# Kernel optimization log

Hardware: AMD Instinct MI355X
Metric: run time of the kernel (lower is better)

The kernel has to match this reference:

```python
import jax, jax.numpy as jnp
import numpy as np

N = 100000
E = 3200000
IN_CH = 512
H1 = 16


def setup_inputs() -> dict:
    key = jax.random.key(0)
    ks = jax.random.split(key, 9)
    x = jax.random.normal(ks[0], (N, IN_CH), dtype=jnp.float32)
    edge_index = jax.random.randint(ks[1], (2, E), 0, N, dtype=jnp.int64)
    # GCNConv params: weight [in, out], bias [out]
    def glorot(k, fan_in, fan_out):
        lim = (6.0 / (fan_in + fan_out)) ** 0.5
        return jax.random.uniform(k, (fan_in, fan_out), jnp.float32, -lim, lim)
    W1 = glorot(ks[2], IN_CH, H1)
    b1 = jnp.zeros((H1,), jnp.float32)
    W2 = glorot(ks[3], H1, H1)
    b2 = jnp.zeros((H1,), jnp.float32)
    W3 = glorot(ks[4], H1, 1)
    b3 = jnp.zeros((1,), jnp.float32)
    return {"x": x, "edge_index": edge_index, "W1": W1, "b1": b1,
            "W2": W2, "b2": b2, "W3": W3, "b3": b3}


def _gcn_conv(x, W, b, src, dst, deg_isqrt):
    # GCNConv: h = X W; out = D^-1/2 (A + I) D^-1/2 h + b
    h = x @ W  # [N, out]
    norm = deg_isqrt[src] * deg_isqrt[dst]  # [E]
    msg = h[src] * norm[:, None]  # gather + scale
    agg = jax.ops.segment_sum(msg, dst, num_segments=N)  # scatter-add
    agg = agg + h * (deg_isqrt * deg_isqrt)[:, None]  # self-loop term
    return agg + b


def reference(x, edge_index, W1, b1, W2, b2, W3, b3):
    src, dst = edge_index[0], edge_index[1]
    # degree of A + I, counted on destination nodes (symmetric norm)
    deg = jax.ops.segment_sum(jnp.ones((E,), jnp.float32), dst, num_segments=N) + 1.0
    deg_isqrt = jax.lax.rsqrt(deg)
    h = _gcn_conv(x, W1, b1, src, dst, deg_isqrt)
    h = jax.nn.relu(h)  # dropout is identity at eval
    h = _gcn_conv(h, W2, b2, src, dst, deg_isqrt)
    h = jax.nn.relu(h)
    out = _gcn_conv(h, W3, b3, src, dst, deg_isqrt)
    return out
```

## Files before the change

kernel.cpp:

```cpp
#include <hip/hip_runtime.h>
#include <hip/hip_bf16.h>

static constexpr int N_NODES = 100000;
static constexpr int N_EDGES = 3200000;
static constexpr int IN_CH = 512;
static constexpr int H = 16;
static constexpr int TB = 256;

static constexpr int BN = 256;
static constexpr int NB = (N_NODES + BN - 1) / BN;
static constexpr int CAP = 8960;
static constexpr int CAP2 = CAP + 3 * BN;
static constexpr int CHUNK = 8192;
static constexpr int GRID_SC = (N_EDGES + CHUNK - 1) / CHUNK;
static constexpr int NBLK64 = (N_NODES + 63) / 64;

__global__ void k_init(int* __restrict__ gcur) {
  int b = blockIdx.x * blockDim.x + threadIdx.x;
  if (b < NB) gcur[b] = b * CAP;
}

__global__ void k_cscatter(const int* __restrict__ ei, int* __restrict__ gcur,
                           int* __restrict__ ebuf) {
  __shared__ int cnt[NB];
  __shared__ int gofs[NB];
  int t = threadIdx.x;
  int c0 = blockIdx.x * CHUNK;
  int c1 = min(c0 + CHUNK, N_EDGES);
  for (int b = t; b < NB; b += TB) cnt[b] = 0;
  __syncthreads();
  for (int j = c0 + t; j < c1; j += TB) atomicAdd(&cnt[ei[N_EDGES + j] >> 8], 1);
  __syncthreads();
  for (int b = t; b < NB; b += TB)
    if (cnt[b] > 0) gofs[b] = atomicAdd(&gcur[b], cnt[b]);
  __syncthreads();
  for (int j = c0 + t; j < c1; j += TB) {
    int s = ei[j];
    int d = ei[N_EDGES + j];
    int slot = atomicAdd(&gofs[d >> 8], 1);
    ebuf[slot] = ((d & 255) << 17) | s;
  }
}

__global__ void k_bsort(const int* __restrict__ gcur, const int* __restrict__ ebuf,
                        int* __restrict__ ebuf2, int* __restrict__ nrs,
                        int* __restrict__ nend, float* __restrict__ disq) {
  __shared__ int cnt[BN];
  __shared__ int pre[BN];
  __shared__ int cur[BN];
  int b = blockIdx.x, t = threadIdx.x;
  cnt[t] = 0;
  __syncthreads();
  int beg = b * CAP, end = gcur[b];
  for (int j = beg + t; j < end; j += TB) atomicAdd(&cnt[ebuf[j] >> 17], 1);
  __syncthreads();
  int myc = cnt[t];
  int ac = (myc + 3) & ~3;
  pre[t] = ac;
  __syncthreads();
  for (int off = 1; off < TB; off <<= 1) {
    int v = (t >= off) ? pre[t - off] : 0;
    __syncthreads();
    pre[t] += v;
    __syncthreads();
  }
  int start = b * CAP2 + ((t == 0) ? 0 : pre[t - 1]);
  cur[t] = start;
  int node = b * BN + t;
  if (node < N_NODES) {
    nrs[node] = start;
    nend[node] = start + ac;
    disq[node] = 1.0f / sqrtf((float)myc + 1.0f);
    for (int j = start + myc; j < start + ac; j++) ebuf2[j] = N_NODES;
  }
  __syncthreads();
  for (int j = beg + t; j < end; j += TB) {
    int p = ebuf[j];
    int slot = atomicAdd(&cur[p >> 17], 1);
    ebuf2[slot] = p & 0x1FFFF;
  }
}

__global__ void k_gemm1(const float* __restrict__ x, const float* __restrict__ W,
                        const float* __restrict__ disq,
                        float* __restrict__ hloA, float* __restrict__ hhiA,
                        float* __restrict__ hloB, float* __restrict__ hhiB,
                        float* __restrict__ hs3) {
  int r = blockIdx.x * blockDim.x + threadIdx.x;
  if (r > N_NODES) return;
  if (r == N_NODES) {
    float4 z = make_float4(0.f, 0.f, 0.f, 0.f);
    ((float4*)(hloA + (size_t)r * 8))[0] = z;
    ((float4*)(hloA + (size_t)r * 8))[1] = z;
    ((float4*)(hhiA + (size_t)r * 8))[0] = z;
    ((float4*)(hhiA + (size_t)r * 8))[1] = z;
    ((float4*)(hloB + (size_t)r * 8))[0] = z;
    ((float4*)(hloB + (size_t)r * 8))[1] = z;
    ((float4*)(hhiB + (size_t)r * 8))[0] = z;
    ((float4*)(hhiB + (size_t)r * 8))[1] = z;
    hs3[r] = 0.f;
    return;
  }
  const float4* xr = (const float4*)(x + (size_t)r * IN_CH);
  float acc[H];
#pragma unroll
  for (int c = 0; c < H; c++) acc[c] = 0.f;
  for (int k4 = 0; k4 < IN_CH / 4; k4++) {
    float4 xv = xr[k4];
    const float* wr = W + k4 * 4 * H;
    float xs[4] = {xv.x, xv.y, xv.z, xv.w};
#pragma unroll
    for (int j = 0; j < 4; j++) {
#pragma unroll
      for (int c = 0; c < H; c++) acc[c] = fmaf(xs[j], wr[j * H + c], acc[c]);
    }
  }
  float dn = disq[r];
  float4* lo = (float4*)(hloA + (size_t)r * 8);
  float4* hi = (float4*)(hhiA + (size_t)r * 8);
  lo[0] = make_float4(acc[0] * dn, acc[1] * dn, acc[2] * dn, acc[3] * dn);
  lo[1] = make_float4(acc[4] * dn, acc[5] * dn, acc[6] * dn, acc[7] * dn);
  hi[0] = make_float4(acc[8] * dn, acc[9] * dn, acc[10] * dn, acc[11] * dn);
  hi[1] = make_float4(acc[12] * dn, acc[13] * dn, acc[14] * dn, acc[15] * dn);
}

__global__ void k_gath_mid(const int* __restrict__ nrs, const int* __restrict__ nend,
                           const int* __restrict__ ebuf2, const float* __restrict__ disq,
                           const float* __restrict__ inlo, const float* __restrict__ inhi,
                           const float* __restrict__ W2, const float* __restrict__ bias,
                           float* __restrict__ outlo, float* __restrict__ outhi) {
  __shared__ float agg[64 * 16];
  __shared__ float w[256];
  int b = blockIdx.x, t = threadIdx.x;
  w[t] = W2[t];
  int grp = t >> 3, lane = t & 7;
#pragma unroll
  for (int ph = 0; ph < 2; ph++) {
    const float* hs = ph ? inhi : inlo;
#pragma unroll
    for (int k = 0; k < 2; k++) {
      int node = b * 64 + grp * 2 + k;
      if (node < N_NODES) {
        int beg = nrs[node], endp = nend[node];
        float acc = 0.f;
        for (int j = beg; j < endp; j += 4) {
          int4 s = *(const int4*)(ebuf2 + j);
          float a0 = hs[(size_t)s.x * 8 + lane];
          float a1 = hs[(size_t)s.y * 8 + lane];
          float a2 = hs[(size_t)s.z * 8 + lane];
          float a3 = hs[(size_t)s.w * 8 + lane];
          acc += (a0 + a1) + (a2 + a3);
        }
        float dn = disq[node];
        agg[(grp * 2 + k) * 16 + ph * 8 + lane] =
            fmaf(acc + hs[(size_t)node * 8 + lane], dn, bias[ph * 8 + lane]);
      }
    }
  }
  __syncthreads();
  int nl = t >> 2, q = t & 3;
  int node = b * 64 + nl;
  if (node < N_NODES) {
    float o0 = 0.f, o1 = 0.f, o2 = 0.f, o3 = 0.f;
#pragma unroll
    for (int c4 = 0; c4 < 4; c4++) {
      float4 av = *(const float4*)(agg + nl * 16 + c4 * 4);
      float vs[4] = {av.x, av.y, av.z, av.w};
#pragma unroll
      for (int i2 = 0; i2 < 4; i2++) {
        float v = fmaxf(vs[i2], 0.f);
        const float* wr = w + (c4 * 4 + i2) * 16 + q * 4;
        o0 = fmaf(v, wr[0], o0);
        o1 = fmaf(v, wr[1], o1);
        o2 = fmaf(v, wr[2], o2);
        o3 = fmaf(v, wr[3], o3);
      }
    }
    float dn = disq[node];
    float4 r = make_float4(o0 * dn, o1 * dn, o2 * dn, o3 * dn);
    if (q < 2) *(float4*)(outlo + (size_t)node * 8 + q * 4) = r;
    else *(float4*)(outhi + (size_t)node * 8 + (q - 2) * 4) = r;
  }
}

__global__ void k_gath_last(const int* __restrict__ nrs, const int* __restrict__ nend,
                            const int* __restrict__ ebuf2, const float* __restrict__ disq,
                            const float* __restrict__ inlo, const float* __restrict__ inhi,
                            const float* __restrict__ W3, const float* __restrict__ bias,
                            float* __restrict__ hs3) {
  __shared__ float agg[64 * 16];
  __shared__ float w3[16];
  int b = blockIdx.x, t = threadIdx.x;
  if (t < 16) w3[t] = W3[t];
  int grp = t >> 3, lane = t & 7;
#pragma unroll
  for (int ph = 0; ph < 2; ph++) {
    const float* hs = ph ? inhi : inlo;
#pragma unroll
    for (int k = 0; k < 2; k++) {
      int node = b * 64 + grp * 2 + k;
      if (node < N_NODES) {
        int beg = nrs[node], endp = nend[node];
        float acc = 0.f;
        for (int j = beg; j < endp; j += 4) {
          int4 s = *(const int4*)(ebuf2 + j);
          float a0 = hs[(size_t)s.x * 8 + lane];
          float a1 = hs[(size_t)s.y * 8 + lane];
          float a2 = hs[(size_t)s.z * 8 + lane];
          float a3 = hs[(size_t)s.w * 8 + lane];
          acc += (a0 + a1) + (a2 + a3);
        }
        float dn = disq[node];
        agg[(grp * 2 + k) * 16 + ph * 8 + lane] =
            fmaf(acc + hs[(size_t)node * 8 + lane], dn, bias[ph * 8 + lane]);
      }
    }
  }
  __syncthreads();
  int nl = t >> 2, q = t & 3;
  int node = b * 64 + nl;
  if (node < N_NODES) {
    float4 av = *(const float4*)(agg + nl * 16 + q * 4);
    float o = fmaxf(av.x, 0.f) * w3[q * 4 + 0];
    o = fmaf(fmaxf(av.y, 0.f), w3[q * 4 + 1], o);
    o = fmaf(fmaxf(av.z, 0.f), w3[q * 4 + 2], o);
    o = fmaf(fmaxf(av.w, 0.f), w3[q * 4 + 3], o);
    o += __shfl_xor(o, 1);
    o += __shfl_xor(o, 2);
    if (q == 0) hs3[node] = o * disq[node];
  }
}

__global__ void k_gath1(const int* __restrict__ nrs, const int* __restrict__ nend,
                        const int* __restrict__ ebuf2, const float* __restrict__ disq,
                        const float* __restrict__ hs3, const float* __restrict__ bias,
                        float* __restrict__ out) {
  int b = blockIdx.x, t = threadIdx.x;
  int nl = t >> 2, lane = t & 3;
  int node = b * 64 + nl;
  if (node >= N_NODES) return;
  int beg = nrs[node], endp = nend[node];
  float acc = 0.f;
  for (int j = beg + 4 * lane; j < endp; j += 16) {
    int4 s = *(const int4*)(ebuf2 + j);
    acc += (hs3[s.x] + hs3[s.y]) + (hs3[s.z] + hs3[s.w]);
  }
  acc += __shfl_xor(acc, 1);
  acc += __shfl_xor(acc, 2);
  if (lane == 0) out[node] = fmaf(acc + hs3[node], disq[node], bias[0]);
}

extern "C" void kernel_launch(void* const* d_in, const int* in_sizes, int n_in,
                              void* d_out, int out_size, void* d_ws, size_t ws_size,
                              hipStream_t stream) {
  const float* x = (const float*)d_in[0];
  const int* ei = (const int*)d_in[1];
  const float* W1 = (const float*)d_in[2];
  const float* b1 = (const float*)d_in[3];
  const float* W2 = (const float*)d_in[4];
  const float* b2 = (const float*)d_in[5];
  const float* W3 = (const float*)d_in[6];
  const float* b3 = (const float*)d_in[7];
  float* out = (float*)d_out;

  int* ebuf = (int*)d_ws;
  int* ebuf2 = ebuf + (size_t)NB * CAP;
  int* gcur = ebuf2 + (size_t)NB * CAP2;
  int* nrs = gcur + NB;
  int* nend = nrs + N_NODES;
  int pad = (4 - ((NB + 2 * N_NODES) & 3)) & 3;
  float* disq = (float*)(nend + N_NODES + pad);
  float* hloA = disq + N_NODES;
  float* hhiA = hloA + (size_t)(N_NODES + 1) * 8;
  float* hloB = hhiA + (size_t)(N_NODES + 1) * 8;
  float* hhiB = hloB + (size_t)(N_NODES + 1) * 8;
  float* hs3 = hhiB + (size_t)(N_NODES + 1) * 8;

  k_init<<<(NB + 63) / 64, 64, 0, stream>>>(gcur);
  k_cscatter<<<GRID_SC, TB, 0, stream>>>(ei, gcur, ebuf);
  k_bsort<<<NB, TB, 0, stream>>>(gcur, ebuf, ebuf2, nrs, nend, disq);

  k_gemm1<<<(N_NODES + 64) / 64, 64, 0, stream>>>(x, W1, disq, hloA, hhiA, hloB, hhiB, hs3);
  k_gath_mid<<<NBLK64, TB, 0, stream>>>(nrs, nend, ebuf2, disq, hloA, hhiA, W2, b1, hloB, hhiB);
  k_gath_last<<<NBLK64, TB, 0, stream>>>(nrs, nend, ebuf2, disq, hloB, hhiB, W3, b2, hs3);
  k_gath1<<<NBLK64, TB, 0, stream>>>(nrs, nend, ebuf2, disq, hs3, b3, out);
}
```

Before: 552.3 us.

## Store 16-wide features contiguously and gather float4 per lane in one pass

Replaces the split lo/hi 8-float feature arrays with a single contiguous 16-float row per node. The gather kernels now have 4 lanes per node, each loading a float4 per neighbor in one pass, instead of 8 lanes doing scalar loads over two phases. Each neighbor row becomes one 64-byte access, and the edge list is walked once instead of twice. The last layer no longer stages results in shared memory or synchronises. In exchange each thread handles more work per edge, with fewer threads per node and less parallelism per edge list.

Result: no change. 557.2 us (+0.9%).

```diff
diff --git a/kernel.cpp b/kernel.cpp
--- a/kernel.cpp
+++ b/kernel.cpp
@@ -83,21 +83,16 @@
 
 __global__ void k_gemm1(const float* __restrict__ x, const float* __restrict__ W,
                         const float* __restrict__ disq,
-                        float* __restrict__ hloA, float* __restrict__ hhiA,
-                        float* __restrict__ hloB, float* __restrict__ hhiB,
+                        float* __restrict__ hA, float* __restrict__ hB,
                         float* __restrict__ hs3) {
   int r = blockIdx.x * blockDim.x + threadIdx.x;
   if (r > N_NODES) return;
+  float4* oa = (float4*)(hA + (size_t)r * 16);
   if (r == N_NODES) {
     float4 z = make_float4(0.f, 0.f, 0.f, 0.f);
-    ((float4*)(hloA + (size_t)r * 8))[0] = z;
-    ((float4*)(hloA + (size_t)r * 8))[1] = z;
-    ((float4*)(hhiA + (size_t)r * 8))[0] = z;
-    ((float4*)(hhiA + (size_t)r * 8))[1] = z;
-    ((float4*)(hloB + (size_t)r * 8))[0] = z;
-    ((float4*)(hloB + (size_t)r * 8))[1] = z;
-    ((float4*)(hhiB + (size_t)r * 8))[0] = z;
-    ((float4*)(hhiB + (size_t)r * 8))[1] = z;
+    float4* ob = (float4*)(hB + (size_t)r * 16);
+#pragma unroll
+    for (int i = 0; i < 4; i++) { oa[i] = z; ob[i] = z; }
     hs3[r] = 0.f;
     return;
   }
@@ -116,55 +111,53 @@
     }
   }
   float dn = disq[r];
-  float4* lo = (float4*)(hloA + (size_t)r * 8);
-  float4* hi = (float4*)(hhiA + (size_t)r * 8);
-  lo[0] = make_float4(acc[0] * dn, acc[1] * dn, acc[2] * dn, acc[3] * dn);
-  lo[1] = make_float4(acc[4] * dn, acc[5] * dn, acc[6] * dn, acc[7] * dn);
-  hi[0] = make_float4(acc[8] * dn, acc[9] * dn, acc[10] * dn, acc[11] * dn);
-  hi[1] = make_float4(acc[12] * dn, acc[13] * dn, acc[14] * dn, acc[15] * dn);
+  oa[0] = make_float4(acc[0] * dn, acc[1] * dn, acc[2] * dn, acc[3] * dn);
+  oa[1] = make_float4(acc[4] * dn, acc[5] * dn, acc[6] * dn, acc[7] * dn);
+  oa[2] = make_float4(acc[8] * dn, acc[9] * dn, acc[10] * dn, acc[11] * dn);
+  oa[3] = make_float4(acc[12] * dn, acc[13] * dn, acc[14] * dn, acc[15] * dn);
 }
 
 __global__ void k_gath_mid(const int* __restrict__ nrs, const int* __restrict__ nend,
                            const int* __restrict__ ebuf2, const float* __restrict__ disq,
-                           const float* __restrict__ inlo, const float* __restrict__ inhi,
-                           const float* __restrict__ W2, const float* __restrict__ bias,
-                           float* __restrict__ outlo, float* __restrict__ outhi) {
-  __shared__ float agg[64 * 16];
+                           const float* __restrict__ hin, const float* __restrict__ W2,
+                           const float* __restrict__ bias, float* __restrict__ hout) {
+  __shared__ float agg[64 * 20];
   __shared__ float w[256];
   int b = blockIdx.x, t = threadIdx.x;
   w[t] = W2[t];
-  int grp = t >> 3, lane = t & 7;
-#pragma unroll
-  for (int ph = 0; ph < 2; ph++) {
-    const float* hs = ph ? inhi : inlo;
-#pragma unroll
-    for (int k = 0; k < 2; k++) {
-      int node = b * 64 + grp * 2 + k;
-      if (node < N_NODES) {
-        int beg = nrs[node], endp = nend[node];
-        float acc = 0.f;
-        for (int j = beg; j < endp; j += 4) {
-          int4 s = *(const int4*)(ebuf2 + j);
-          float a0 = hs[(size_t)s.x * 8 + lane];
-          float a1 = hs[(size_t)s.y * 8 + lane];
-          float a2 = hs[(size_t)s.z * 8 + lane];
-          float a3 = hs[(size_t)s.w * 8 + lane];
-          acc += (a0 + a1) + (a2 + a3);
-        }
-        float dn = disq[node];
-        agg[(grp * 2 + k) * 16 + ph * 8 + lane] =
-            fmaf(acc + hs[(size_t)node * 8 + lane], dn, bias[ph * 8 + lane]);
-      }
-    }
-  }
-  __syncthreads();
   int nl = t >> 2, q = t & 3;
   int node = b * 64 + nl;
+  const float4* hin4 = (const float4*)hin;
+  if (node < N_NODES) {
+    int beg = nrs[node], endp = nend[node];
+    float4 acc = make_float4(0.f, 0.f, 0.f, 0.f);
+    for (int j = beg; j < endp; j += 4) {
+      int4 s = *(const int4*)(ebuf2 + j);
+      float4 a0 = hin4[s.x * 4 + q];
+      float4 a1 = hin4[s.y * 4 + q];
+      float4 a2 = hin4[s.z * 4 + q];
+      float4 a3 = hin4[s.w * 4 + q];
+      acc.x += (a0.x + a1.x) + (a2.x + a3.x);
+      acc.y += (a0.y + a1.y) + (a2.y + a3.y);
+      acc.z += (a0.z + a1.z) + (a2.z + a3.z);
+      acc.w += (a0.w + a1.w) + (a2.w + a3.w);
+    }
+    float4 sf = hin4[node * 4 + q];
+    float dn = disq[node];
+    float4 bi = *(const float4*)(bias + q * 4);
+    float4 r;
+    r.x = fmaf(acc.x + sf.x, dn, bi.x);
+    r.y = fmaf(acc.y + sf.y, dn, bi.y);
+    r.z = fmaf(acc.z + sf.z, dn, bi.z);
+    r.w = fmaf(acc.w + sf.w, dn, bi.w);
+    *(float4*)(agg + nl * 20 + q * 4) = r;
+  }
+  __syncthreads();
   if (node < N_NODES) {
     float o0 = 0.f, o1 = 0.f, o2 = 0.f, o3 = 0.f;
 #pragma unroll
     for (int c4 = 0; c4 < 4; c4++) {
-      float4 av = *(const float4*)(agg + nl * 16 + c4 * 4);
+      float4 av = *(const float4*)(agg + nl * 20 + c4 * 4);
       float vs[4] = {av.x, av.y, av.z, av.w};
 #pragma unroll
       for (int i2 = 0; i2 < 4; i2++) {
@@ -177,58 +170,48 @@
       }
     }
     float dn = disq[node];
-    float4 r = make_float4(o0 * dn, o1 * dn, o2 * dn, o3 * dn);
-    if (q < 2) *(float4*)(outlo + (size_t)node * 8 + q * 4) = r;
-    else *(float4*)(outhi + (size_t)node * 8 + (q - 2) * 4) = r;
+    *(float4*)(hout + (size_t)node * 16 + q * 4) =
+        make_float4(o0 * dn, o1 * dn, o2 * dn, o3 * dn);
   }
 }
 
 __global__ void k_gath_last(const int* __restrict__ nrs, const int* __restrict__ nend,
                             const int* __restrict__ ebuf2, const float* __restrict__ disq,
-                            const float* __restrict__ inlo, const float* __restrict__ inhi,
-                            const float* __restrict__ W3, const float* __restrict__ bias,
-                            float* __restrict__ hs3) {
-  __shared__ float agg[64 * 16];
-  __shared__ float w3[16];
-  int b = blockIdx.x, t = threadIdx.x;
-  if (t < 16) w3[t] = W3[t];
-  int grp = t >> 3, lane = t & 7;
-#pragma unroll
-  for (int ph = 0; ph < 2; ph++) {
-    const float* hs = ph ? inhi : inlo;
-#pragma unroll
-    for (int k = 0; k < 2; k++) {
-      int node = b * 64 + grp * 2 + k;
-      if (node < N_NODES) {
-        int beg = nrs[node], endp = nend[node];
-        float acc = 0.f;
-        for (int j = beg; j < endp; j += 4) {
-          int4 s = *(const int4*)(ebuf2 + j);
-          float a0 = hs[(size_t)s.x * 8 + lane];
-          float a1 = hs[(size_t)s.y * 8 + lane];
-          float a2 = hs[(size_t)s.z * 8 + lane];
-          float a3 = hs[(size_t)s.w * 8 + lane];
-          acc += (a0 + a1) + (a2 + a3);
-        }
-        float dn = disq[node];
-        agg[(grp * 2 + k) * 16 + ph * 8 + lane] =
-            fmaf(acc + hs[(size_t)node * 8 + lane], dn, bias[ph * 8 + lane]);
-      }
-    }
-  }
-  __syncthreads();
+                            const float* __restrict__ hin, const float* __restrict__ W3,
+                            const float* __restrict__ bias, float* __restrict__ hs3) {
+  int b = blockIdx.x, t = threadIdx.x;
   int nl = t >> 2, q = t & 3;
   int node = b * 64 + nl;
-  if (node < N_NODES) {
-    float4 av = *(const float4*)(agg + nl * 16 + q * 4);
-    float o = fmaxf(av.x, 0.f) * w3[q * 4 + 0];
-    o = fmaf(fmaxf(av.y, 0.f), w3[q * 4 + 1], o);
-    o = fmaf(fmaxf(av.z, 0.f), w3[q * 4 + 2], o);
-    o = fmaf(fmaxf(av.w, 0.f), w3[q * 4 + 3], o);
-    o += __shfl_xor(o, 1);
-    o += __shfl_xor(o, 2);
-    if (q == 0) hs3[node] = o * disq[node];
-  }
+  if (node >= N_NODES) return;
+  const float4* hin4 = (const float4*)hin;
+  int beg = nrs[node], endp = nend[node];
+  float4 acc = make_float4(0.f, 0.f, 0.f, 0.f);
+  for (int j = beg; j < endp; j += 4) {
+    int4 s = *(const int4*)(ebuf2 + j);
+    float4 a0 = hin4[s.x * 4 + q];
+    float4 a1 = hin4[s.y * 4 + q];
+    float4 a2 = hin4[s.z * 4 + q];
+    float4 a3 = hin4[s.w * 4 + q];
+    acc.x += (a0.x + a1.x) + (a2.x + a3.x);
+    acc.y += (a0.y + a1.y) + (a2.y + a3.y);
+    acc.z += (a0.z + a1.z) + (a2.z + a3.z);
+    acc.w += (a0.w + a1.w) + (a2.w + a3.w);
+  }
+  float4 sf = hin4[node * 4 + q];
+  float dn = disq[node];
+  float4 bi = *(const float4*)(bias + q * 4);
+  float4 w3 = *(const float4*)(W3 + q * 4);
+  float v0 = fmaxf(fmaf(acc.x + sf.x, dn, bi.x), 0.f);
+  float v1 = fmaxf(fmaf(acc.y + sf.y, dn, bi.y), 0.f);
+  float v2 = fmaxf(fmaf(acc.z + sf.z, dn, bi.z), 0.f);
+  float v3 = fmaxf(fmaf(acc.w + sf.w, dn, bi.w), 0.f);
+  float o = v0 * w3.x;
+  o = fmaf(v1, w3.y, o);
+  o = fmaf(v2, w3.z, o);
+  o = fmaf(v3, w3.w, o);
+  o += __shfl_xor(o, 1);
+  o += __shfl_xor(o, 2);
+  if (q == 0) hs3[node] = o * dn;
 }
 
 __global__ void k_gath1(const int* __restrict__ nrs, const int* __restrict__ nend,
@@ -270,18 +253,16 @@
   int* nend = nrs + N_NODES;
   int pad = (4 - ((NB + 2 * N_NODES) & 3)) & 3;
   float* disq = (float*)(nend + N_NODES + pad);
-  float* hloA = disq + N_NODES;
-  float* hhiA = hloA + (size_t)(N_NODES + 1) * 8;
-  float* hloB = hhiA + (size_t)(N_NODES + 1) * 8;
-  float* hhiB = hloB + (size_t)(N_NODES + 1) * 8;
-  float* hs3 = hhiB + (size_t)(N_NODES + 1) * 8;
+  float* hA = disq + N_NODES;
+  float* hB = hA + (size_t)(N_NODES + 1) * 16;
+  float* hs3 = hB + (size_t)(N_NODES + 1) * 16;
 
   k_init<<<(NB + 63) / 64, 64, 0, stream>>>(gcur);
   k_cscatter<<<GRID_SC, TB, 0, stream>>>(ei, gcur, ebuf);
   k_bsort<<<NB, TB, 0, stream>>>(gcur, ebuf, ebuf2, nrs, nend, disq);
 
-  k_gemm1<<<(N_NODES + 64) / 64, 64, 0, stream>>>(x, W1, disq, hloA, hhiA, hloB, hhiB, hs3);
-  k_gath_mid<<<NBLK64, TB, 0, stream>>>(nrs, nend, ebuf2, disq, hloA, hhiA, W2, b1, hloB, hhiB);
-  k_gath_last<<<NBLK64, TB, 0, stream>>>(nrs, nend, ebuf2, disq, hloB, hhiB, W3, b2, hs3);
+  k_gemm1<<<(N_NODES + 64) / 64, 64, 0, stream>>>(x, W1, disq, hA, hB, hs3);
+  k_gath_mid<<<NBLK64, TB, 0, stream>>>(nrs, nend, ebuf2, disq, hA, W2, b1, hB);
+  k_gath_last<<<NBLK64, TB, 0, stream>>>(nrs, nend, ebuf2, disq, hB, W3, b2, hs3);
   k_gath1<<<NBLK64, TB, 0, stream>>>(nrs, nend, ebuf2, disq, hs3, b3, out);
 }
```
